# Kernel optimization log

Measured on AMD Instinct MI355X. Metric: run time of the kernel, lower is better.

Reference implementation:

```python
import jax, jax.numpy as jnp
import numpy as np

B = 1024          # batch
L = 200           # max_len (history length)
DIM = 64          # args.dim
ITEM_NUM = 100000 # vocab; table has ITEM_NUM+1 rows, row 0 = padding
NEG = -1e15       # mask additive constant used by the original module


def setup_inputs() -> dict:
    key = jax.random.key(0)
    k1, k2, k3, k4, k5 = jax.random.split(key, 5)
    log_seqs = jax.random.randint(k1, (B, L), 0, ITEM_NUM + 1)          # item ids, 0 = pad
    pred = jax.random.randint(k2, (B, 1), 0, ITEM_NUM + 1)              # gather targets
    item_emb = jax.random.normal(k3, (ITEM_NUM + 1, DIM), jnp.float32) * 0.02
    item_emb = item_emb.at[0].set(0.0)                                  # padding_idx=0
    attn_key = jax.random.uniform(k4, (1, DIM), jnp.float32)            # self.key (torch.rand init)
    pos_emb = jax.random.normal(k5, (L, DIM), jnp.float32) * 0.02       # positional table
    return {"log_seqs": log_seqs, "pred": pred, "item_emb": item_emb,
            "attn_key": attn_key, "pos_emb": pos_emb}


def reference(log_seqs, pred, item_emb, attn_key, pos_emb):
    dim = item_emb.shape[1]
    mask = log_seqs != 0                                  # [B, L] True where valid
    # log2feats (model='P2MAMO', dropout p=0 -> identity)
    seqs = item_emb[log_seqs] * jnp.sqrt(jnp.float32(dim))  # [B, L, D]
    seqs = seqs + pos_emb[None, :, :]
    seqs = seqs * mask[..., None]                         # zero out padded positions
    # single-query dot-product attention pooling with learned key
    sim = jnp.einsum('bld,d->bl', seqs, attn_key[0])      # (q*k).sum(-1)
    sim = sim + jnp.where(mask, 0.0, NEG)                 # sim + (~mask)*-1e15
    attn = jax.nn.softmax(sim, axis=-1)                   # [B, L]
    Q = jnp.einsum('bld,bl->bd', seqs, attn)              # [B, D]
    # training path (isEval=False): full-vocab logits -> softmax -> gather
    logits = Q @ item_emb.T                               # [B, V+1]
    probs = jax.nn.softmax(logits, axis=-1)
    pos_logits = jnp.take_along_axis(probs, pred, axis=1) # [B, 1]
    return pos_logits
```

## Files before the change

kernel.cpp:

```cpp
#include <hip/hip_runtime.h>
#include <math.h>

#define B_TOT   1024
#define L_SEQ   200
#define DIM     64
#define VOCAB   100001
#define NEG_BIG (-1e15f)
#define SEQ_ST16 66
#define LOG2E   1.4426950408889634f

typedef __bf16 bf16x8 __attribute__((ext_vector_type(8)));
typedef float  f32x4  __attribute__((ext_vector_type(4)));

static __device__ __forceinline__ float fast_exp2(float x) {
    return __builtin_amdgcn_exp2f(x);
}

__global__ __launch_bounds__(256) void pool_kernel(
    const int*   __restrict__ log_seqs,
    const float* __restrict__ item_emb,
    const float* __restrict__ attn_key,
    const float* __restrict__ pos_emb,
    float*       __restrict__ Q,
    __bf16*      __restrict__ Qb,
    __bf16*      __restrict__ Eb)
{
    const int b    = blockIdx.x;
    const int t    = threadIdx.x;
    const int wave = t >> 6;
    const int lane = t & 63;

    __shared__ unsigned short s_seq16[L_SEQ][SEQ_ST16];
    __shared__ float s_attn[L_SEQ];
    __shared__ float s_red[4];
    __shared__ float s_q[4][DIM];

    float sim = -INFINITY;
    if (t < L_SEQ) {
        const int id = log_seqs[(long)b * L_SEQ + t];
        if (id == 0) {
            sim = NEG_BIG;
            const ushort2 z = make_ushort2(0, 0);
            #pragma unroll
            for (int i = 0; i < DIM / 2; ++i)
                *(ushort2*)&s_seq16[t][2 * i] = z;
        } else {
            float acc = 0.f;
            const float4* e4 = (const float4*)(item_emb + (long)id * DIM);
            const float4* p4 = (const float4*)(pos_emb + t * DIM);
            #pragma unroll
            for (int i = 0; i < DIM / 4; ++i) {
                const float4 e = e4[i];
                const float4 p = p4[i];
                float4 f;
                f.x = fmaf(8.f, e.x, p.x);
                f.y = fmaf(8.f, e.y, p.y);
                f.z = fmaf(8.f, e.z, p.z);
                f.w = fmaf(8.f, e.w, p.w);
                const __bf16 h0 = (__bf16)f.x, h1 = (__bf16)f.y;
                const __bf16 h2 = (__bf16)f.z, h3 = (__bf16)f.w;
                ushort2 u0, u1;
                u0.x = __builtin_bit_cast(unsigned short, h0);
                u0.y = __builtin_bit_cast(unsigned short, h1);
                u1.x = __builtin_bit_cast(unsigned short, h2);
                u1.y = __builtin_bit_cast(unsigned short, h3);
                *(ushort2*)&s_seq16[t][4 * i]     = u0;
                *(ushort2*)&s_seq16[t][4 * i + 2] = u1;
                acc += f.x * attn_key[4*i+0] + f.y * attn_key[4*i+1]
                     + f.z * attn_key[4*i+2] + f.w * attn_key[4*i+3];
            }
            sim = acc;
        }
    }

    float m = sim;
    #pragma unroll
    for (int off = 32; off > 0; off >>= 1) m = fmaxf(m, __shfl_xor(m, off));
    if (lane == 0) s_red[wave] = m;
    __syncthreads();
    m = fmaxf(fmaxf(s_red[0], s_red[1]), fmaxf(s_red[2], s_red[3]));
    __syncthreads();

    float p = (t < L_SEQ) ? __expf(sim - m) : 0.f;
    if (t < L_SEQ) s_attn[t] = p;
    float ls = p;
    #pragma unroll
    for (int off = 32; off > 0; off >>= 1) ls += __shfl_xor(ls, off);
    if (lane == 0) s_red[wave] = ls;
    __syncthreads();
    const float inv = 1.0f / (s_red[0] + s_red[1] + s_red[2] + s_red[3]);

    float q = 0.f;
    const int l0 = wave * (L_SEQ / 4);
    #pragma unroll 2
    for (int l = l0; l < l0 + (L_SEQ / 4); ++l) {
        const unsigned int ui = (unsigned int)s_seq16[l][lane] << 16;
        q = fmaf(s_attn[l], __builtin_bit_cast(float, ui), q);
    }
    s_q[wave][lane] = q;
    __syncthreads();

    if (t < DIM) {
        const float qq = (s_q[0][t] + s_q[1][t] + s_q[2][t] + s_q[3][t]) * inv;
        Q[b * DIM + t]  = qq;
        Qb[b * DIM + t] = (__bf16)(qq * LOG2E);
    }

    {
        const long n8 = ((long)VOCAB * DIM) / 8;
        for (long g = (long)b * 256 + t; g < n8; g += (long)gridDim.x * 256) {
            const long i = g * 8;
            const float4 f0 = ((const float4*)(item_emb + i))[0];
            const float4 f1 = ((const float4*)(item_emb + i))[1];
            bf16x8 o;
            o[0] = (__bf16)f0.x; o[1] = (__bf16)f0.y; o[2] = (__bf16)f0.z; o[3] = (__bf16)f0.w;
            o[4] = (__bf16)f1.x; o[5] = (__bf16)f1.y; o[6] = (__bf16)f1.z; o[7] = (__bf16)f1.w;
            *(bf16x8*)(Eb + i) = o;
        }
    }
}

#define NC        128
#define NBG       8
#define VT_TOTAL  6251
#define VT_FULL   6250

__global__ __launch_bounds__(256) void logits_mfma(
    const __bf16* __restrict__ Eb,
    const __bf16* __restrict__ Qb,
    float*        __restrict__ partials)
{
    const int bid   = blockIdx.x;
    const int xcd   = bid & 7;
    const int idx   = bid >> 3;
    const int chunk = xcd + 8 * (idx >> 3);
    const int bg    = idx & 7;
    const int wave  = threadIdx.x >> 6;
    const int lane  = threadIdx.x & 63;
    const int r16   = lane & 15;
    const int hi    = lane >> 4;

    __shared__ float s_part[4][128];

    bf16x8 a[8][2];
    #pragma unroll
    for (int t = 0; t < 8; ++t)
        #pragma unroll
        for (int s = 0; s < 2; ++s)
            a[t][s] = *(const bf16x8*)(Qb + ((bg*128 + t*16 + r16) * DIM) + s*32 + hi*8);

    const int per    = (VT_TOTAL + NC - 1) / NC;
    const int vt_end = min((chunk + 1) * per, VT_TOTAL);
    int vt = chunk * per + wave;

    float ssum[8][4];
    #pragma unroll
    for (int t = 0; t < 8; ++t)
        #pragma unroll
        for (int r = 0; r < 4; ++r) ssum[t][r] = 0.f;

    #define LOADB(dst0, dst1, vti) do {                                       \
        const int _row = min((vti) * 16 + r16, VOCAB - 1);                    \
        const __bf16* _p = Eb + (size_t)_row * DIM + hi * 8;                  \
        dst0 = *(const bf16x8*)_p;                                            \
        dst1 = *(const bf16x8*)(_p + 32);                                     \
    } while (0)

    bf16x8 b0, b1, d0, d1;
    LOADB(b0, b1, vt);
    LOADB(d0, d1, vt + 4);

    while (vt < vt_end) {
        const bf16x8 c00 = b0, c01 = b1, c10 = d0, c11 = d1;
        const int v0 = vt, v1 = vt + 4;
        vt += 8;
        LOADB(b0, b1, vt);
        LOADB(d0, d1, vt + 4);

        if (v0 < VT_FULL) {
            #pragma unroll
            for (int t = 0; t < 8; ++t) {
                f32x4 acc = {0.f, 0.f, 0.f, 0.f};
                acc = __builtin_amdgcn_mfma_f32_16x16x32_bf16(a[t][0], c00, acc, 0, 0, 0);
                acc = __builtin_amdgcn_mfma_f32_16x16x32_bf16(a[t][1], c01, acc, 0, 0, 0);
                #pragma unroll
                for (int r = 0; r < 4; ++r) ssum[t][r] += fast_exp2(acc[r]);
            }
        } else {
            const bool valid = (v0 * 16 + r16) < VOCAB;
            #pragma unroll
            for (int t = 0; t < 8; ++t) {
                f32x4 acc = {0.f, 0.f, 0.f, 0.f};
                acc = __builtin_amdgcn_mfma_f32_16x16x32_bf16(a[t][0], c00, acc, 0, 0, 0);
                acc = __builtin_amdgcn_mfma_f32_16x16x32_bf16(a[t][1], c01, acc, 0, 0, 0);
                #pragma unroll
                for (int r = 0; r < 4; ++r) ssum[t][r] += valid ? fast_exp2(acc[r]) : 0.f;
            }
        }
        if (v1 < vt_end) {
            if (v1 < VT_FULL) {
                #pragma unroll
                for (int t = 0; t < 8; ++t) {
                    f32x4 acc = {0.f, 0.f, 0.f, 0.f};
                    acc = __builtin_amdgcn_mfma_f32_16x16x32_bf16(a[t][0], c10, acc, 0, 0, 0);
                    acc = __builtin_amdgcn_mfma_f32_16x16x32_bf16(a[t][1], c11, acc, 0, 0, 0);
                    #pragma unroll
                    for (int r = 0; r < 4; ++r) ssum[t][r] += fast_exp2(acc[r]);
                }
            } else {
                const bool valid = (v1 * 16 + r16) < VOCAB;
                #pragma unroll
                for (int t = 0; t < 8; ++t) {
                    f32x4 acc = {0.f, 0.f, 0.f, 0.f};
                    acc = __builtin_amdgcn_mfma_f32_16x16x32_bf16(a[t][0], c10, acc, 0, 0, 0);
                    acc = __builtin_amdgcn_mfma_f32_16x16x32_bf16(a[t][1], c11, acc, 0, 0, 0);
                    #pragma unroll
                    for (int r = 0; r < 4; ++r) ssum[t][r] += valid ? fast_exp2(acc[r]) : 0.f;
                }
            }
        }
    }
    #undef LOADB

    #pragma unroll
    for (int t = 0; t < 8; ++t)
        #pragma unroll
        for (int r = 0; r < 4; ++r) {
            float v = ssum[t][r];
            v += __shfl_xor(v, 1);
            v += __shfl_xor(v, 2);
            v += __shfl_xor(v, 4);
            v += __shfl_xor(v, 8);
            ssum[t][r] = v;
        }

    if (r16 == 0) {
        #pragma unroll
        for (int t = 0; t < 8; ++t)
            #pragma unroll
            for (int r = 0; r < 4; ++r)
                s_part[wave][t * 16 + hi * 4 + r] = ssum[t][r];
    }
    __syncthreads();

    if (threadIdx.x < 128) {
        const int i = threadIdx.x;
        const float v = s_part[0][i] + s_part[1][i] + s_part[2][i] + s_part[3][i];
        partials[(size_t)chunk * B_TOT + bg * 128 + i] = v;
    }
}

__global__ __launch_bounds__(256) void finalize_kernel(
    const float* __restrict__ Q,
    const float* __restrict__ item_emb,
    const int*   __restrict__ pred,
    const float* __restrict__ partials,
    float*       __restrict__ out)
{
    const int b = blockIdx.x * 256 + threadIdx.x;

    float S = 0.f;
    for (int c = 0; c < NC; ++c)
        S += partials[(size_t)c * B_TOT + b];

    const int pv = pred[b];
    float acc = 0.f;
    const float4* e4 = (const float4*)(item_emb + (long)pv * DIM);
    const float4* q4 = (const float4*)(Q + b * DIM);
    #pragma unroll
    for (int i = 0; i < DIM / 4; ++i) {
        const float4 e = e4[i];
        const float4 q = q4[i];
        acc += e.x*q.x + e.y*q.y + e.z*q.z + e.w*q.w;
    }
    out[b] = __expf(acc) / S;
}

extern "C" void kernel_launch(void* const* d_in, const int* in_sizes, int n_in,
                              void* d_out, int out_size, void* d_ws, size_t ws_size,
                              hipStream_t stream)
{
    const int*   log_seqs = (const int*)  d_in[0];
    const int*   pred     = (const int*)  d_in[1];
    const float* item_emb = (const float*)d_in[2];
    const float* attn_key = (const float*)d_in[3];
    const float* pos_emb  = (const float*)d_in[4];
    float*       out      = (float*)d_out;

    char* ws = (char*)d_ws;
    __bf16* Eb       = (__bf16*)ws;
    __bf16* Qb       = (__bf16*)(ws + (size_t)VOCAB * DIM * 2);
    float*  Qf       = (float*) (ws + (size_t)VOCAB * DIM * 2 + (size_t)B_TOT * DIM * 2);
    float*  partials = (float*) ((char*)Qf + (size_t)B_TOT * DIM * 4);

    pool_kernel<<<B_TOT, 256, 0, stream>>>(log_seqs, item_emb, attn_key, pos_emb, Qf, Qb, Eb);
    logits_mfma<<<NBG * NC, 256, 0, stream>>>(Eb, Qb, partials);
    finalize_kernel<<<B_TOT / 256, 256, 0, stream>>>(Qf, item_emb, pred, partials, out);
}
```

Measured before the change: 64.67 us.

## Split batch tiles across waves and double vocab chunks in logits kernel

The logits MFMA kernel now gives each wave 2 batch tiles (32 rows) instead of all 8. Each block's 4 waves walk the same contiguous 25-tile vocab range rather than striding it, and the chunk count rises from 128 to 256. This removes the shared-memory cross-wave reduction and the barrier, cuts register use, and should allow more occupancy and parallelism. In exchange, each embedding tile is loaded by all 4 waves, so there are fewer MFMAs per load, and the finalize step must sum twice as many partials.

```diff
diff --git a/kernel.cpp b/kernel.cpp
--- a/kernel.cpp
+++ b/kernel.cpp
@@ -120,10 +120,11 @@
     }
 }
 
-#define NC        128
+#define NC        256
 #define NBG       8
 #define VT_TOTAL  6251
 #define VT_FULL   6250
+#define VT_PER    25
 
 __global__ __launch_bounds__(256) void logits_mfma(
     const __bf16* __restrict__ Eb,
@@ -140,22 +141,19 @@
     const int r16   = lane & 15;
     const int hi    = lane >> 4;
 
-    __shared__ float s_part[4][128];
-
-    bf16x8 a[8][2];
-    #pragma unroll
-    for (int t = 0; t < 8; ++t)
+    bf16x8 a[2][2];
+    #pragma unroll
+    for (int t = 0; t < 2; ++t)
         #pragma unroll
         for (int s = 0; s < 2; ++s)
-            a[t][s] = *(const bf16x8*)(Qb + ((bg*128 + t*16 + r16) * DIM) + s*32 + hi*8);
-
-    const int per    = (VT_TOTAL + NC - 1) / NC;
-    const int vt_end = min((chunk + 1) * per, VT_TOTAL);
-    int vt = chunk * per + wave;
-
-    float ssum[8][4];
-    #pragma unroll
-    for (int t = 0; t < 8; ++t)
+            a[t][s] = *(const bf16x8*)(Qb + ((bg*128 + (wave*2 + t)*16 + r16) * DIM) + s*32 + hi*8);
+
+    int vt           = chunk * VT_PER;
+    const int vt_end = min(vt + VT_PER, VT_TOTAL);
+
+    float ssum[2][4];
+    #pragma unroll
+    for (int t = 0; t < 2; ++t)
         #pragma unroll
         for (int r = 0; r < 4; ++r) ssum[t][r] = 0.f;
 
@@ -168,62 +166,38 @@
 
     bf16x8 b0, b1, d0, d1;
     LOADB(b0, b1, vt);
-    LOADB(d0, d1, vt + 4);
-
-    while (vt < vt_end) {
-        const bf16x8 c00 = b0, c01 = b1, c10 = d0, c11 = d1;
-        const int v0 = vt, v1 = vt + 4;
-        vt += 8;
-        LOADB(b0, b1, vt);
-        LOADB(d0, d1, vt + 4);
-
-        if (v0 < VT_FULL) {
-            #pragma unroll
-            for (int t = 0; t < 8; ++t) {
+    LOADB(d0, d1, vt + 1);
+
+    for (; vt < vt_end; ++vt) {
+        const bf16x8 c0 = b0, c1 = b1;
+        b0 = d0; b1 = d1;
+        LOADB(d0, d1, vt + 2);
+
+        if (vt < VT_FULL) {
+            #pragma unroll
+            for (int t = 0; t < 2; ++t) {
                 f32x4 acc = {0.f, 0.f, 0.f, 0.f};
-                acc = __builtin_amdgcn_mfma_f32_16x16x32_bf16(a[t][0], c00, acc, 0, 0, 0);
-                acc = __builtin_amdgcn_mfma_f32_16x16x32_bf16(a[t][1], c01, acc, 0, 0, 0);
+                acc = __builtin_amdgcn_mfma_f32_16x16x32_bf16(a[t][0], c0, acc, 0, 0, 0);
+                acc = __builtin_amdgcn_mfma_f32_16x16x32_bf16(a[t][1], c1, acc, 0, 0, 0);
                 #pragma unroll
                 for (int r = 0; r < 4; ++r) ssum[t][r] += fast_exp2(acc[r]);
             }
         } else {
-            const bool valid = (v0 * 16 + r16) < VOCAB;
-            #pragma unroll
-            for (int t = 0; t < 8; ++t) {
+            const bool valid = (vt * 16 + r16) < VOCAB;
+            #pragma unroll
+            for (int t = 0; t < 2; ++t) {
                 f32x4 acc = {0.f, 0.f, 0.f, 0.f};
-                acc = __builtin_amdgcn_mfma_f32_16x16x32_bf16(a[t][0], c00, acc, 0, 0, 0);
-                acc = __builtin_amdgcn_mfma_f32_16x16x32_bf16(a[t][1], c01, acc, 0, 0, 0);
+                acc = __builtin_amdgcn_mfma_f32_16x16x32_bf16(a[t][0], c0, acc, 0, 0, 0);
+                acc = __builtin_amdgcn_mfma_f32_16x16x32_bf16(a[t][1], c1, acc, 0, 0, 0);
                 #pragma unroll
                 for (int r = 0; r < 4; ++r) ssum[t][r] += valid ? fast_exp2(acc[r]) : 0.f;
             }
         }
-        if (v1 < vt_end) {
-            if (v1 < VT_FULL) {
-                #pragma unroll
-                for (int t = 0; t < 8; ++t) {
-                    f32x4 acc = {0.f, 0.f, 0.f, 0.f};
-                    acc = __builtin_amdgcn_mfma_f32_16x16x32_bf16(a[t][0], c10, acc, 0, 0, 0);
-                    acc = __builtin_amdgcn_mfma_f32_16x16x32_bf16(a[t][1], c11, acc, 0, 0, 0);
-                    #pragma unroll
-                    for (int r = 0; r < 4; ++r) ssum[t][r] += fast_exp2(acc[r]);
-                }
-            } else {
-                const bool valid = (v1 * 16 + r16) < VOCAB;
-                #pragma unroll
-                for (int t = 0; t < 8; ++t) {
-                    f32x4 acc = {0.f, 0.f, 0.f, 0.f};
-                    acc = __builtin_amdgcn_mfma_f32_16x16x32_bf16(a[t][0], c10, acc, 0, 0, 0);
-                    acc = __builtin_amdgcn_mfma_f32_16x16x32_bf16(a[t][1], c11, acc, 0, 0, 0);
-                    #pragma unroll
-                    for (int r = 0; r < 4; ++r) ssum[t][r] += valid ? fast_exp2(acc[r]) : 0.f;
-                }
-            }
-        }
     }
     #undef LOADB
 
     #pragma unroll
-    for (int t = 0; t < 8; ++t)
+    for (int t = 0; t < 2; ++t)
         #pragma unroll
         for (int r = 0; r < 4; ++r) {
             float v = ssum[t][r];
@@ -236,17 +210,12 @@
 
     if (r16 == 0) {
         #pragma unroll
-        for (int t = 0; t < 8; ++t)
-            #pragma unroll
-            for (int r = 0; r < 4; ++r)
-                s_part[wave][t * 16 + hi * 4 + r] = ssum[t][r];
-    }
-    __syncthreads();
-
-    if (threadIdx.x < 128) {
-        const int i = threadIdx.x;
-        const float v = s_part[0][i] + s_part[1][i] + s_part[2][i] + s_part[3][i];
-        partials[(size_t)chunk * B_TOT + bg * 128 + i] = v;
+        for (int t = 0; t < 2; ++t)
+            #pragma unroll
+            for (int r = 0; r < 4; ++r) {
+                const int row = bg * 128 + (wave*2 + t) * 16 + hi * 4 + r;
+                partials[(size_t)chunk * B_TOT + row] = ssum[t][r];
+            }
     }
 }
 
```

Result: slower. 96.05 us (+48.5%).
